# Optimization experiments

Measured on AMD Instinct MI355X. Metric: run time of the kernel, lower is better.

The kernel has to match this reference:

```python
import jax, jax.numpy as jnp
import numpy as np

EPS = 1e-4  # BatchNorm2d eps from source


def binarize(x):
    # brevitas 1-bit quant: sign(x) with sign(0)=+1; straight-through (clipped) estimator
    y = jnp.clip(x, -1.0, 1.0)
    q = jnp.where(x >= 0, 1.0, -1.0).astype(x.dtype)
    return y + jax.lax.stop_gradient(q - y)


def bn(x, g, b, m, v):
    inv = g / jnp.sqrt(v + EPS)
    return x * inv[None, :, None, None] + (b - m * inv)[None, :, None, None]


def conv(x, w, pad):
    return jax.lax.conv_general_dilated(
        x, w, window_strides=(1, 1), padding=[(pad, pad), (pad, pad)],
        dimension_numbers=('NCHW', 'OIHW', 'NCHW'))


def conv_mod(x, w1, bn1, w3, bn3):
    # conv1x1(binary W) -> BN -> binarize act -> conv3x3(binary W) -> BN -> binarize act
    x = conv(x, binarize(w1), 0)
    x = binarize(bn(x, *bn1))
    x = conv(x, binarize(w3), 1)
    x = binarize(bn(x, *bn3))
    return x


def maxpool2(x):
    return jax.lax.reduce_window(x, -jnp.inf, jax.lax.max,
                                 (1, 1, 2, 2), (1, 1, 2, 2), 'VALID')


def setup_inputs() -> dict:
    key = jax.random.key(0)
    ks = jax.random.split(key, 24)
    B, Cin, down, up, H, W = 16, 256, 64, 256, 56, 56
    d = {
        'x':   jax.random.normal(ks[0], (B, Cin, H, W), jnp.float32),
        'w11': jax.random.normal(ks[1], (down, Cin, 1, 1), jnp.float32) * 0.1,
        'w31': jax.random.normal(ks[2], (up, down, 3, 3), jnp.float32) * 0.1,
        'w12': jax.random.normal(ks[3], (down, up, 1, 1), jnp.float32) * 0.1,
        'w32': jax.random.normal(ks[4], (up, down, 3, 3), jnp.float32) * 0.1,
    }
    # BatchNorm params (inference stats): gamma, beta, running mean, running var
    for i, (tag, c) in enumerate([('11', down), ('31', up), ('12', down), ('32', up)]):
        d['g' + tag] = jax.random.uniform(ks[5 + 4 * i], (c,), jnp.float32, 0.5, 1.5)
        d['b' + tag] = jax.random.normal(ks[6 + 4 * i], (c,), jnp.float32) * 0.1
        d['m' + tag] = jax.random.normal(ks[7 + 4 * i], (c,), jnp.float32) * 0.1
        d['v' + tag] = jax.random.uniform(ks[8 + 4 * i], (c,), jnp.float32, 0.5, 1.5)
    return d


def reference(x, w11, w31, w12, w32,
              g11, b11, m11, v11, g31, b31, m31, v31,
              g12, b12, m12, v12, g32, b32, m32, v32):
    h = conv_mod(x, w11, (g11, b11, m11, v11), w31, (g31, b31, m31, v31))
    r = conv_mod(h, w12, (g12, b12, m12, v12), w32, (g32, b32, m32, v32))
    s = binarize(h + r)          # quant_add: re-binarize the residual sum
    return maxpool2(s)           # MaxPool2d(2)
```

## Files before the change

### kernel.cpp

```cpp
#include <hip/hip_runtime.h>
#include <stdint.h>

#pragma clang fp contract(off)


#define HW_   3136
#define NPIX  50176

#define OFF_W31B   0
#define OFF_W12B   18432
#define OFF_W32B   20480
#define OFF_IV11   38912
#define OFF_IV31   39424
#define OFF_IV12   41472
#define OFF_IV32   41984
#define OFF_SGNT   44032
#define OFF_A1     109568
#define OFF_A2     510976
#define OFF_H      912384
#define OFF_S      2518016

__device__ inline float2 mk_ivbt(float g, float b, float m, float v) {
    float inv  = __fdiv_rn(g, __fsqrt_rn(__fadd_rn(v, 1e-4f)));
    float beta = __fsub_rn(b, __fmul_rn(m, inv));
    return make_float2(inv, beta);
}

__global__ __launch_bounds__(256) void k0_all(
    const float* __restrict__ w11, const float* __restrict__ w31,
    const float* __restrict__ w12, const float* __restrict__ w32,
    const float* __restrict__ g11, const float* __restrict__ b11,
    const float* __restrict__ m11, const float* __restrict__ v11,
    const float* __restrict__ g31, const float* __restrict__ b31,
    const float* __restrict__ m31, const float* __restrict__ v31,
    const float* __restrict__ g12, const float* __restrict__ b12,
    const float* __restrict__ m12, const float* __restrict__ v12,
    const float* __restrict__ g32, const float* __restrict__ b32,
    const float* __restrict__ m32, const float* __restrict__ v32,
    uint64_t* __restrict__ W31b, uint64_t* __restrict__ W12b,
    uint64_t* __restrict__ W32b,
    float2* __restrict__ iv11, float2* __restrict__ iv31,
    float2* __restrict__ iv12, float2* __restrict__ iv32,
    float* __restrict__ sgnT)
{
    int blk = blockIdx.x;
    if (blk < 1216) {
        int wid = blk * 4 + (threadIdx.x >> 6);
        int l = threadIdx.x & 63;
        if (wid < 2304) {
            int co = wid / 9, tap = wid % 9;
            uint64_t bits = __ballot(w31[(co * 64 + l) * 9 + tap] >= 0.f);
            if (l == 0) W31b[wid] = bits;
        } else if (wid < 4608) {
            int i = wid - 2304;
            int co = i / 9, tap = i % 9;
            uint64_t bits = __ballot(w32[(co * 64 + l) * 9 + tap] >= 0.f);
            if (l == 0) W32b[i] = bits;
        } else if (wid < 4864) {
            int i = wid - 4608;
            int co = i >> 2, k = i & 3;
            uint64_t bits = __ballot(w12[co * 256 + k * 64 + l] >= 0.f);
            if (l == 0) W12b[i] = bits;
        }
    } else if (blk < 1219) {
        int i = (blk - 1216) * 256 + threadIdx.x;
        if (i < 64)        iv11[i]       = mk_ivbt(g11[i],       b11[i],       m11[i],       v11[i]);
        else if (i < 320)  iv31[i - 64]  = mk_ivbt(g31[i - 64],  b31[i - 64],  m31[i - 64],  v31[i - 64]);
        else if (i < 384)  iv12[i - 320] = mk_ivbt(g12[i - 320], b12[i - 320], m12[i - 320], v12[i - 320]);
        else if (i < 640)  iv32[i - 384] = mk_ivbt(g32[i - 384], b32[i - 384], m32[i - 384], v32[i - 384]);
    } else {
        int t = (blk - 1219) * 256 + threadIdx.x;
        int j = t >> 8, ci = t & 255;
        sgnT[ci * 64 + j] = (w11[t] >= 0.f) ? 1.0f : -1.0f;
    }
}

__global__ __launch_bounds__(256) void k1_conv1(
    const float* __restrict__ x, const float* __restrict__ sgnT,
    const float2* __restrict__ ivbt, unsigned char* __restrict__ A1)
{
    const int l = threadIdx.x & 63;
    const int wv = __builtin_amdgcn_readfirstlane(threadIdx.x >> 6);
    const int blk = blockIdx.x;
    const int half = blk & 1;
    const int g = half * 4 + wv;
    const int P = (blk >> 1) * 256 + l * 4;
    const int bl = P / HW_;
    const int pxl = P - bl * HW_;
    const float* xp = x + (size_t)bl * (256 * HW_) + pxl;
    const float* sg = sgnT + g * 8;

    float acc[8][4];
#pragma unroll
    for (int j = 0; j < 8; ++j)
#pragma unroll
        for (int p = 0; p < 4; ++p) acc[j][p] = 0.0f;

    for (int ci = 0; ci < 256; ci += 8) {
        float4 xv[8];
#pragma unroll
        for (int k = 0; k < 8; ++k)
            xv[k] = *(const float4*)(xp + (size_t)(ci + k) * HW_);
#pragma unroll
        for (int k = 0; k < 8; ++k) {
            const float* s = sg + (ci + k) * 64;
#pragma unroll
            for (int j = 0; j < 8; ++j) {
                acc[j][0] = __builtin_fmaf(s[j], xv[k].x, acc[j][0]);
                acc[j][1] = __builtin_fmaf(s[j], xv[k].y, acc[j][1]);
                acc[j][2] = __builtin_fmaf(s[j], xv[k].z, acc[j][2]);
                acc[j][3] = __builtin_fmaf(s[j], xv[k].w, acc[j][3]);
            }
        }
    }

    unsigned bp0 = 0, bp1 = 0, bp2 = 0, bp3 = 0;
#pragma unroll
    for (int j = 0; j < 8; ++j) {
        float2 ib = ivbt[g * 8 + j];
        bp0 |= (__fadd_rn(__fmul_rn(acc[j][0], ib.x), ib.y) >= 0.0f) ? (1u << j) : 0u;
        bp1 |= (__fadd_rn(__fmul_rn(acc[j][1], ib.x), ib.y) >= 0.0f) ? (1u << j) : 0u;
        bp2 |= (__fadd_rn(__fmul_rn(acc[j][2], ib.x), ib.y) >= 0.0f) ? (1u << j) : 0u;
        bp3 |= (__fadd_rn(__fmul_rn(acc[j][3], ib.x), ib.y) >= 0.0f) ? (1u << j) : 0u;
    }
    unsigned char* a = A1 + (size_t)P * 8 + g;
    a[0]  = (unsigned char)bp0;
    a[8]  = (unsigned char)bp1;
    a[16] = (unsigned char)bp2;
    a[24] = (unsigned char)bp3;
}

template <bool MERGE, bool DO_K3>
__global__ __launch_bounds__(256) void k_conv3b(
    const uint64_t* __restrict__ A, const uint64_t* __restrict__ Wb,
    const float2* __restrict__ ivbt, const uint64_t* __restrict__ Hin,
    uint64_t* __restrict__ Out,
    const uint64_t* __restrict__ W12b, const float2* __restrict__ iv12,
    unsigned short* __restrict__ A2)
{
    __shared__ uint64_t tile[4 * 58];
    __shared__ uint64_t sh4[4][64];
    const int l = threadIdx.x & 63;
    const int wv = threadIdx.x >> 6;
    const int chunk = blockIdx.x;
    const int b = chunk / 49;
    const int hw0 = (chunk % 49) * 64;
    const int r0 = hw0 / 56;
    const int o  = hw0 % 56;
    const int rfirst = r0 - 1;

    {
        int idx = threadIdx.x;
        if (idx < 4 * 58) {
            int rr = idx / 58, cc = idx % 58;
            int gh = rfirst + rr, gw = cc - 1;
            uint64_t v = 0;
            if ((unsigned)gh < 56u && (unsigned)gw < 56u)
                v = A[b * HW_ + gh * 56 + gw];
            tile[idx] = v;
        }
    }

    const int co = wv * 64 + l;
    uint64_t wp[9];
    int c64[9];
#pragma unroll
    for (int t = 0; t < 9; ++t) {
        wp[t] = Wb[co * 9 + t];
        c64[t] = 64 - 2 * (int)__popcll(wp[t]);
    }
    const float2 ib = ivbt[co];

    __syncthreads();

    uint64_t res = 0;
    for (int p = 0; p < 64; ++p) {
        const int inrow2 = (p >= 56 - o) ? 1 : 0;
        const int w = o + p - (inrow2 ? 56 : 0);
        const int row = r0 + inrow2;
        const int rbase = inrow2 * 58;

        int s = 0;
#pragma unroll
        for (int dr = 0; dr < 3; ++dr)
#pragma unroll
            for (int dc = 0; dc < 3; ++dc) {
                uint64_t a = tile[rbase + dr * 58 + w + dc];
                s += (int)__popcll(a ^ wp[dr * 3 + dc]);
            }
        int y = 576 - 2 * s;

        unsigned um = 0;
        if (row == 0)  um |= 0x007u;
        if (row == 55) um |= 0x1C0u;
        if (w == 0)    um |= 0x049u;
        if (w == 55)   um |= 0x124u;
        if (um) {
#pragma unroll
            for (int t = 0; t < 9; ++t)
                if ((um >> t) & 1u) y -= c64[t];
        }

        float val = __fadd_rn(__fmul_rn((float)y, ib.x), ib.y);
        uint64_t word = __ballot(val >= 0.0f);
        res = (l == p) ? word : res;
    }

    size_t oidx = (size_t)wv * NPIX + (size_t)(b * HW_) + hw0 + l;
    if (MERGE) res |= Hin[oidx];
    Out[oidx] = res;

    if (DO_K3) {
        sh4[wv][l] = res;
        __syncthreads();
        uint64_t h0 = sh4[0][l], h1 = sh4[1][l], h2 = sh4[2][l], h3 = sh4[3][l];
        unsigned bits16 = 0;
#pragma unroll
        for (int jj = 0; jj < 16; ++jj) {
            int cq = wv * 16 + jj;
            const uint64_t* wq = W12b + cq * 4;
            int s = (int)(__popcll(h0 ^ wq[0]) + __popcll(h1 ^ wq[1]) +
                          __popcll(h2 ^ wq[2]) + __popcll(h3 ^ wq[3]));
            int y = 256 - 2 * s;
            float2 ibq = iv12[cq];
            float val = __fadd_rn(__fmul_rn((float)y, ibq.x), ibq.y);
            bits16 |= (val >= 0.0f) ? (1u << jj) : 0u;
        }
        A2[(size_t)(b * HW_ + hw0 + l) * 4 + wv] = (unsigned short)bits16;
    }
}

__global__ __launch_bounds__(256) void k4b_pool(
    const uint64_t* __restrict__ S, float* __restrict__ out)
{
    int o = blockIdx.x * 256 + threadIdx.x;
    int ow = o % 28;
    int t = o / 28;
    int oh = t % 28; t /= 28;
    int co = t & 255;
    int b  = t >> 8;
    int k = co >> 6, j = co & 63;
    const uint64_t* Sk = S + (size_t)k * NPIX + (size_t)(b * HW_) + (2 * oh) * 56 + 2 * ow;
    uint64_t s = Sk[0] | Sk[1] | Sk[56] | Sk[57];
    out[o] = ((s >> j) & 1) ? 1.0f : -1.0f;
}

extern "C" void kernel_launch(void* const* d_in, const int* in_sizes, int n_in,
                              void* d_out, int out_size, void* d_ws, size_t ws_size,
                              hipStream_t stream)
{
    const float* x   = (const float*)d_in[0];
    const float* w11 = (const float*)d_in[1];
    const float* w31 = (const float*)d_in[2];
    const float* w12 = (const float*)d_in[3];
    const float* w32 = (const float*)d_in[4];
    const float* g11 = (const float*)d_in[5];
    const float* b11 = (const float*)d_in[6];
    const float* m11 = (const float*)d_in[7];
    const float* v11 = (const float*)d_in[8];
    const float* g31 = (const float*)d_in[9];
    const float* b31 = (const float*)d_in[10];
    const float* m31 = (const float*)d_in[11];
    const float* v31 = (const float*)d_in[12];
    const float* g12 = (const float*)d_in[13];
    const float* b12 = (const float*)d_in[14];
    const float* m12 = (const float*)d_in[15];
    const float* v12 = (const float*)d_in[16];
    const float* g32 = (const float*)d_in[17];
    const float* b32 = (const float*)d_in[18];
    const float* m32 = (const float*)d_in[19];
    const float* v32 = (const float*)d_in[20];

    char* ws = (char*)d_ws;
    uint64_t* W31b = (uint64_t*)(ws + OFF_W31B);
    uint64_t* W12b = (uint64_t*)(ws + OFF_W12B);
    uint64_t* W32b = (uint64_t*)(ws + OFF_W32B);
    float2* iv11 = (float2*)(ws + OFF_IV11);
    float2* iv31 = (float2*)(ws + OFF_IV31);
    float2* iv12 = (float2*)(ws + OFF_IV12);
    float2* iv32 = (float2*)(ws + OFF_IV32);
    float*  sgnT = (float*)(ws + OFF_SGNT);
    uint64_t* A1 = (uint64_t*)(ws + OFF_A1);
    uint64_t* A2 = (uint64_t*)(ws + OFF_A2);
    uint64_t* Hb = (uint64_t*)(ws + OFF_H);
    uint64_t* Sb = (uint64_t*)(ws + OFF_S);

    k0_all<<<dim3(1283), dim3(256), 0, stream>>>(
        w11, w31, w12, w32,
        g11, b11, m11, v11, g31, b31, m31, v31,
        g12, b12, m12, v12, g32, b32, m32, v32,
        W31b, W12b, W32b, iv11, iv31, iv12, iv32, sgnT);

    k1_conv1<<<dim3(392), dim3(256), 0, stream>>>(x, sgnT, iv11, (unsigned char*)A1);

    k_conv3b<false, true><<<dim3(784), dim3(256), 0, stream>>>(
        A1, W31b, iv31, (const uint64_t*)nullptr, Hb,
        W12b, iv12, (unsigned short*)A2);

    k_conv3b<true, false><<<dim3(784), dim3(256), 0, stream>>>(
        A2, W32b, iv32, Hb, Sb,
        (const uint64_t*)nullptr, (const float2*)nullptr, (unsigned short*)nullptr);

    k4b_pool<<<dim3(12544), dim3(256), 0, stream>>>(Sb, (float*)d_out);
}
```

Baseline: 120.2 us.

## Swap binary 3x3 conv mapping to per-pixel lanes with wave-uniform weight loads

The binary 3x3 conv kernel now gives each lane one pixel and loops over the 64 output channels of its wave. Before, each lane owned one output channel and looped over 64 pixels, assembling bits with a ballot per pixel. Weights and BN params are indexed by a readfirstlane wave id, so they can become scalar/uniform loads. Border handling uses precomputed per-tap masks and a valid-tap count instead of per-pixel correction branches. The cost is nine held activation words and masks per lane, and per-iteration weight loads in place of register-resident weights.

Result: faster. 116.0 us, median of 2 (-3.5%).

```diff
diff --git a/kernel.cpp b/kernel.cpp
--- a/kernel.cpp
+++ b/kernel.cpp
@@ -131,7 +131,7 @@
 }
 
 template <bool MERGE, bool DO_K3>
-__global__ __launch_bounds__(256) void k_conv3b(
+__global__ __launch_bounds__(256) void k_conv3c(
     const uint64_t* __restrict__ A, const uint64_t* __restrict__ Wb,
     const float2* __restrict__ ivbt, const uint64_t* __restrict__ Hin,
     uint64_t* __restrict__ Out,
@@ -142,6 +142,7 @@
     __shared__ uint64_t sh4[4][64];
     const int l = threadIdx.x & 63;
     const int wv = threadIdx.x >> 6;
+    const int wvu = __builtin_amdgcn_readfirstlane(wv);
     const int chunk = blockIdx.x;
     const int b = chunk / 49;
     const int hw0 = (chunk % 49) * 64;
@@ -160,64 +161,57 @@
             tile[idx] = v;
         }
     }
-
-    const int co = wv * 64 + l;
-    uint64_t wp[9];
-    int c64[9];
-#pragma unroll
-    for (int t = 0; t < 9; ++t) {
-        wp[t] = Wb[co * 9 + t];
-        c64[t] = 64 - 2 * (int)__popcll(wp[t]);
-    }
-    const float2 ib = ivbt[co];
-
     __syncthreads();
 
-    uint64_t res = 0;
-    for (int p = 0; p < 64; ++p) {
-        const int inrow2 = (p >= 56 - o) ? 1 : 0;
-        const int w = o + p - (inrow2 ? 56 : 0);
-        const int row = r0 + inrow2;
-        const int rbase = inrow2 * 58;
-
+    const int inrow2 = (l >= 56 - o) ? 1 : 0;
+    const int w = o + l - (inrow2 ? 56 : 0);
+    const int row = r0 + inrow2;
+    const int rbase = inrow2 * 58;
+
+    uint64_t a[9], m[9];
+    int nv = 0;
+#pragma unroll
+    for (int dr = 0; dr < 3; ++dr)
+#pragma unroll
+        for (int dc = 0; dc < 3; ++dc) {
+            int t = dr * 3 + dc;
+            a[t] = tile[rbase + dr * 58 + w + dc];
+            bool ok = ((unsigned)(row + dr - 1) < 56u) &&
+                      ((unsigned)(w + dc - 1) < 56u);
+            m[t] = ok ? ~0ull : 0ull;
+            nv += ok;
+        }
+    const int base = 64 * nv;
+
+    const uint64_t* wbase = Wb + wvu * 64 * 9;
+    const float2*   ivb   = ivbt + wvu * 64;
+
+    uint64_t bits = 0;
+#pragma unroll 4
+    for (int jo = 0; jo < 64; ++jo) {
+        const uint64_t* wq = wbase + jo * 9;
         int s = 0;
 #pragma unroll
-        for (int dr = 0; dr < 3; ++dr)
-#pragma unroll
-            for (int dc = 0; dc < 3; ++dc) {
-                uint64_t a = tile[rbase + dr * 58 + w + dc];
-                s += (int)__popcll(a ^ wp[dr * 3 + dc]);
-            }
-        int y = 576 - 2 * s;
-
-        unsigned um = 0;
-        if (row == 0)  um |= 0x007u;
-        if (row == 55) um |= 0x1C0u;
-        if (w == 0)    um |= 0x049u;
-        if (w == 55)   um |= 0x124u;
-        if (um) {
-#pragma unroll
-            for (int t = 0; t < 9; ++t)
-                if ((um >> t) & 1u) y -= c64[t];
-        }
-
+        for (int t = 0; t < 9; ++t)
+            s += (int)__popcll((a[t] ^ wq[t]) & m[t]);
+        int y = base - 2 * s;
+        float2 ib = ivb[jo];
         float val = __fadd_rn(__fmul_rn((float)y, ib.x), ib.y);
-        uint64_t word = __ballot(val >= 0.0f);
-        res = (l == p) ? word : res;
+        bits |= (uint64_t)(val >= 0.0f) << jo;
     }
 
     size_t oidx = (size_t)wv * NPIX + (size_t)(b * HW_) + hw0 + l;
-    if (MERGE) res |= Hin[oidx];
-    Out[oidx] = res;
+    if (MERGE) bits |= Hin[oidx];
+    Out[oidx] = bits;
 
     if (DO_K3) {
-        sh4[wv][l] = res;
+        sh4[wv][l] = bits;
         __syncthreads();
         uint64_t h0 = sh4[0][l], h1 = sh4[1][l], h2 = sh4[2][l], h3 = sh4[3][l];
         unsigned bits16 = 0;
 #pragma unroll
         for (int jj = 0; jj < 16; ++jj) {
-            int cq = wv * 16 + jj;
+            int cq = wvu * 16 + jj;
             const uint64_t* wq = W12b + cq * 4;
             int s = (int)(__popcll(h0 ^ wq[0]) + __popcll(h1 ^ wq[1]) +
                           __popcll(h2 ^ wq[2]) + __popcll(h3 ^ wq[3]));
@@ -293,11 +287,11 @@
 
     k1_conv1<<<dim3(392), dim3(256), 0, stream>>>(x, sgnT, iv11, (unsigned char*)A1);
 
-    k_conv3b<false, true><<<dim3(784), dim3(256), 0, stream>>>(
+    k_conv3c<false, true><<<dim3(784), dim3(256), 0, stream>>>(
         A1, W31b, iv31, (const uint64_t*)nullptr, Hb,
         W12b, iv12, (unsigned short*)A2);
 
-    k_conv3b<true, false><<<dim3(784), dim3(256), 0, stream>>>(
+    k_conv3c<true, false><<<dim3(784), dim3(256), 0, stream>>>(
         A2, W32b, iv32, Hb, Sb,
         (const uint64_t*)nullptr, (const float2*)nullptr, (unsigned short*)nullptr);
 
```
